# Kernel tuning notes

Measured on AMD Instinct MI355X. Metric: run time of the kernel, lower is better.

The kernel has to match this reference:

```python
import jax, jax.numpy as jnp
import numpy as np

B, L, D, N = 2, 2048, 1024, 16
DT_MIN, DT_MAX = 1e-3, 1e-1


def setup_inputs() -> dict:
    key = jax.random.key(0)
    ks = jax.random.split(key, 8)
    u = jax.random.normal(ks[0], (B, L, D), dtype=jnp.float32)
    # torch.nn.Linear weights are (out_features, in_features)
    W_dt = jax.random.normal(ks[1], (D, D), dtype=jnp.float32) * 0.02
    b_dt = jnp.zeros((D,), dtype=jnp.float32)
    W_B = jax.random.normal(ks[2], (D * N, D), dtype=jnp.float32) * 0.02
    b_B = jnp.zeros((D * N,), dtype=jnp.float32)
    W_C = jax.random.normal(ks[3], (D * N, D), dtype=jnp.float32) * 0.02
    b_C = jnp.zeros((D * N,), dtype=jnp.float32)
    # log_A init: log(1..N) broadcast over channels (HiPPO-ish diagonal)
    log_A = jnp.broadcast_to(jnp.log(jnp.arange(1, N + 1, dtype=jnp.float32)), (D, N))
    D_skip = jnp.ones((D,), dtype=jnp.float32)
    lo, hi = float(np.log(DT_MIN)), float(np.log(DT_MAX))
    dt_bias = jax.random.uniform(ks[4], (D,), dtype=jnp.float32) * (hi - lo) + lo
    return {"u": u, "log_A": log_A, "D_skip": D_skip, "dt_bias": dt_bias,
            "W_dt": W_dt, "b_dt": b_dt, "W_B": W_B, "b_B": b_B,
            "W_C": W_C, "b_C": b_C}


def reference(u, log_A, D_skip, dt_bias, W_dt, b_dt, W_B, b_B, W_C, b_C):
    b, l, d = u.shape
    n = log_A.shape[1]
    A = -jnp.exp(log_A)                                   # (d, n), A < 0
    # token-dependent parameters, computed for all timesteps at once
    dt = jax.nn.softplus(u @ W_dt.T + b_dt + dt_bias)     # (b, l, d)
    Bt = (u @ W_B.T + b_B).reshape(b, l, d, n)            # (b, l, d, n)
    Ct = (u @ W_C.T + b_C).reshape(b, l, d, n)            # (b, l, d, n)
    # exact ZOH discretisation
    A_bar = jnp.exp(dt[..., None] * A)                    # (b, l, d, n)
    B_bar = (A_bar - 1.0) / A * Bt                        # (b, l, d, n)
    x_in = B_bar * u[..., None]                           # (b, l, d, n)
    # recurrent scan over time
    def step(h, inp):
        a_t, x_t, c_t = inp                               # each (b, d, n)
        h = a_t * h + x_t
        y_t = jnp.sum(c_t * h, axis=-1)                   # (b, d)
        return h, y_t
    h0 = jnp.zeros((b, d, n), dtype=u.dtype)
    xs = (jnp.moveaxis(A_bar, 1, 0), jnp.moveaxis(x_in, 1, 0), jnp.moveaxis(Ct, 1, 0))
    _, ys = jax.lax.scan(step, h0, xs)                    # ys: (l, b, d)
    y = jnp.moveaxis(ys, 0, 1) + D_skip * u               # (b, l, d)
    return y
```

## Files before the change

kernel.cpp:

```cpp
#include <hip/hip_runtime.h>
#include <hip/hip_bf16.h>
#include <stdint.h>

constexpr int Bb = 2;
constexpr int Ll = 2048;
constexpr int Dd = 1024;
constexpr int Nn = 16;
constexpr int NB = Dd * Nn;
constexpr int SL = 64;
constexpr int NCH = Bb * Dd;
constexpr int KCAT = 3 * Dd;

typedef __bf16 bf16_t;
typedef __bf16 bf16x8 __attribute__((ext_vector_type(8)));
typedef __bf16 bf16x4 __attribute__((ext_vector_type(4)));
typedef float f32x4 __attribute__((ext_vector_type(4)));

__device__ inline void gld_lds16(const void* g, void* l) {
    __builtin_amdgcn_global_load_lds(
        (const __attribute__((address_space(1))) unsigned int*)g,
        (__attribute__((address_space(3))) unsigned int*)l, 16, 0, 0);
}

__global__ __launch_bounds__(256) void cvt_bf16(const float* __restrict__ s,
                                                bf16_t* __restrict__ d, int n4) {
    int i = blockIdx.x * 256 + threadIdx.x;
    const int stride = gridDim.x * 256;
    const float4* s4 = (const float4*)s;
    bf16x4* d4 = (bf16x4*)d;
    for (; i < n4; i += stride) {
        float4 v = s4[i];
        bf16x4 o = {(bf16_t)v.x, (bf16_t)v.y, (bf16_t)v.z, (bf16_t)v.w};
        d4[i] = o;
    }
}

__global__ __launch_bounds__(256) void build_ucat(const float* __restrict__ u,
                                                  bf16_t* __restrict__ ucat,
                                                  bf16_t* __restrict__ ubf) {
    const int i = blockIdx.x * 256 + threadIdx.x;
    const int row = i >> 8;
    const int c = (i & 255) << 2;
    float4 v = ((const float4*)u)[i];
    bf16x4 hi = {(bf16_t)v.x, (bf16_t)v.y, (bf16_t)v.z, (bf16_t)v.w};
    bf16x4 lo = {(bf16_t)(v.x - (float)hi.x), (bf16_t)(v.y - (float)hi.y),
                 (bf16_t)(v.z - (float)hi.z), (bf16_t)(v.w - (float)hi.w)};
    bf16_t* r = ucat + (size_t)row * KCAT;
    *(bf16x4*)(r + c) = hi;
    *(bf16x4*)(r + Dd + c) = lo;
    *(bf16x4*)(r + 2 * Dd + c) = hi;
    *(bf16x4*)(ubf + (size_t)i * 4) = hi;
}

__global__ __launch_bounds__(256) void build_wcat(const float* __restrict__ w,
                                                  bf16_t* __restrict__ wcat) {
    const int i = blockIdx.x * 256 + threadIdx.x;
    const int row = i >> 8;
    const int c = (i & 255) << 2;
    float4 v = ((const float4*)w)[i];
    bf16x4 hi = {(bf16_t)v.x, (bf16_t)v.y, (bf16_t)v.z, (bf16_t)v.w};
    bf16x4 lo = {(bf16_t)(v.x - (float)hi.x), (bf16_t)(v.y - (float)hi.y),
                 (bf16_t)(v.z - (float)hi.z), (bf16_t)(v.w - (float)hi.w)};
    bf16_t* r = wcat + (size_t)row * KCAT;
    *(bf16x4*)(r + c) = hi;
    *(bf16x4*)(r + Dd + c) = hi;
    *(bf16x4*)(r + 2 * Dd + c) = lo;
}

template <int EP, typename OutT>
__global__ __launch_bounds__(256) void gemm_mfma(
    const bf16_t* __restrict__ Abase, int CL, int l0, int K,
    const bf16_t* __restrict__ W, const float* __restrict__ b1,
    const float* __restrict__ b2, OutT* __restrict__ C, int N)
{
    __shared__ bf16_t As[128 * 32];
    __shared__ bf16_t Bs[128 * 32];

    const int tid = threadIdx.x;
    const int bn = blockIdx.x * 128;
    const int rglob = blockIdx.y * 128;
    const int batch = rglob / CL;
    const int rin = rglob % CL;
    const bf16_t* Ap = Abase + ((size_t)batch * Ll + l0 + rin) * K;
    const bf16_t* Wp = W + (size_t)bn * K;
    OutT* Cp = C + (size_t)rglob * N;

    const int sr = tid >> 2;
    const int sc = (tid & 3) << 3;
    char* ldsA = (char*)As + tid * 16;
    char* ldsB = (char*)Bs + tid * 16;

    const int lane = tid & 63;
    const int wid = tid >> 6;
    const int wm = (wid & 1) << 6;
    const int wn = (wid >> 1) << 6;
    const int lr = lane & 15;
    const int lq = lane >> 4;

    f32x4 acc[4][4] = {};

    for (int k0 = 0; k0 < K; k0 += 32) {
        __syncthreads();
        gld_lds16(Ap + (size_t)sr * K + k0 + sc, ldsA);
        gld_lds16(Ap + (size_t)(sr + 64) * K + k0 + sc, ldsA + 4096);
        gld_lds16(Wp + (size_t)sr * K + k0 + sc, ldsB);
        gld_lds16(Wp + (size_t)(sr + 64) * K + k0 + sc, ldsB + 4096);
        __syncthreads();

        bf16x8 af[4], bfr[4];
#pragma unroll
        for (int mi = 0; mi < 4; ++mi)
            af[mi] = *(const bf16x8*)&As[(wm + mi * 16 + lr) * 32 + lq * 8];
#pragma unroll
        for (int ni = 0; ni < 4; ++ni)
            bfr[ni] = *(const bf16x8*)&Bs[(wn + ni * 16 + lr) * 32 + lq * 8];
#pragma unroll
        for (int mi = 0; mi < 4; ++mi)
#pragma unroll
            for (int ni = 0; ni < 4; ++ni)
                acc[mi][ni] = __builtin_amdgcn_mfma_f32_16x16x32_bf16(
                    af[mi], bfr[ni], acc[mi][ni], 0, 0, 0);
    }

#pragma unroll
    for (int ni = 0; ni < 4; ++ni) {
        const int col = bn + wn + ni * 16 + lr;
        const float bc = b1[col] + (EP == 1 ? b2[col] : 0.f);
#pragma unroll
        for (int mi = 0; mi < 4; ++mi)
#pragma unroll
            for (int i = 0; i < 4; ++i) {
                float v = acc[mi][ni][i] + bc;
                if (EP == 1) v = (v > 20.f) ? v : log1pf(__expf(v));
                Cp[(size_t)(wm + mi * 16 + lq * 4 + i) * N + col] = (OutT)v;
            }
    }
}

__global__ __launch_bounds__(512, 4) void gemm_dt(
    const bf16_t* __restrict__ A, int K, const bf16_t* __restrict__ W,
    const float* __restrict__ b1, const float* __restrict__ b2,
    float* __restrict__ C)
{
    extern __shared__ char smem[];
    char* const smA = smem;
    char* const smB = smem + 49152;
    const int tid = threadIdx.x;
    const int bn = blockIdx.x * 128;
    const int row0 = blockIdx.y * 128;
    const bf16_t* Ap = A + (size_t)row0 * K;
    const bf16_t* Wp = W + (size_t)bn * K;
    float* Cp = C + (size_t)row0 * Dd;

    const int lane = tid & 63;
    const int wid = tid >> 6;
    const int wr = wid >> 2;
    const int wc = wid & 3;
    const int lr = lane & 15;
    const int lq = lane >> 4;
    const int NT = K >> 6;

    const int c0 = tid, c1 = tid + 512;
    const int r0 = c0 >> 3, r1 = c1 >> 3;
    const int kb0 = ((c0 & 7) << 3) ^ ((r0 & 7) << 3);
    const int kb1 = ((c1 & 7) << 3) ^ ((r1 & 7) << 3);

    auto stageA = [&](int tt, int slot) {
        gld_lds16(Ap + (size_t)r0 * K + tt * 64 + kb0, smA + slot * 16384 + c0 * 16);
        gld_lds16(Ap + (size_t)r1 * K + tt * 64 + kb1, smA + slot * 16384 + c1 * 16);
    };
    auto stageB = [&](int tt, int slot) {
        gld_lds16(Wp + (size_t)r0 * K + tt * 64 + kb0, smB + slot * 16384 + c0 * 16);
        gld_lds16(Wp + (size_t)r1 * K + tt * 64 + kb1, smB + slot * 16384 + c1 * 16);
    };

    stageA(0, 0); stageB(0, 0); stageA(1, 1); stageB(1, 1);
    asm volatile("s_waitcnt vmcnt(4)" ::: "memory");
    __builtin_amdgcn_s_barrier();

    f32x4 acc[4][2] = {};
    const int xsw = (lr & 7) << 4;
    int as_rd = 0, as_wr = 2;

    for (int t = 0; t < NT; ++t) {
        const char* Ard = smA + as_rd * 16384;
        const char* Brd = smB + (t & 1) * 16384;

        bf16x8 bfr[2][2];
#pragma unroll
        for (int p = 0; p < 4; ++p) {
            if (p == 0 && t + 2 < NT) stageA(t + 2, as_wr);
            if (p == 2 && t + 2 < NT) stageB(t + 2, (t & 1));

            if (p == 0) {
#pragma unroll
                for (int ks = 0; ks < 2; ++ks)
#pragma unroll
                    for (int ni = 0; ni < 2; ++ni)
                        bfr[ks][ni] = *(const bf16x8*)(Brd +
                            (wc * 32 + ni * 16 + lr) * 128 +
                            ((ks * 64 + lq * 16) ^ xsw));
            }
            bf16x8 ak0 = *(const bf16x8*)(Ard +
                (wr * 64 + p * 16 + lr) * 128 + ((lq * 16) ^ xsw));
            bf16x8 ak1 = *(const bf16x8*)(Ard +
                (wr * 64 + p * 16 + lr) * 128 + ((64 + lq * 16) ^ xsw));

            __builtin_amdgcn_s_barrier();
            __builtin_amdgcn_s_setprio(1);
#pragma unroll
            for (int ni = 0; ni < 2; ++ni) {
                acc[p][ni] = __builtin_amdgcn_mfma_f32_16x16x32_bf16(
                    bfr[0][ni], ak0, acc[p][ni], 0, 0, 0);
                acc[p][ni] = __builtin_amdgcn_mfma_f32_16x16x32_bf16(
                    bfr[1][ni], ak1, acc[p][ni], 0, 0, 0);
            }
            __builtin_amdgcn_s_setprio(0);
            if (p == 3) {
                if (t + 2 < NT)
                    asm volatile("s_waitcnt vmcnt(4)" ::: "memory");
                else if (t + 1 < NT)
                    asm volatile("s_waitcnt vmcnt(0)" ::: "memory");
            }
            __builtin_amdgcn_s_barrier();
        }
        ++as_rd; if (as_rd == 3) as_rd = 0;
        ++as_wr; if (as_wr == 3) as_wr = 0;
    }

#pragma unroll
    for (int ni = 0; ni < 2; ++ni) {
        const int col = bn + wc * 32 + ni * 16 + lq * 4;
        const float4 ba = *(const float4*)&b1[col];
        const float4 bb = *(const float4*)&b2[col];
        const float bc[4] = {ba.x + bb.x, ba.y + bb.y, ba.z + bb.z, ba.w + bb.w};
#pragma unroll
        for (int mi = 0; mi < 4; ++mi) {
            const int row = wr * 64 + mi * 16 + lr;
            f32x4 v;
#pragma unroll
            for (int i = 0; i < 4; ++i) {
                float tv = acc[mi][ni][i] + bc[i];
                v[i] = (tv > 20.f) ? tv : log1pf(__expf(tv));
            }
            *(f32x4*)(Cp + (size_t)row * Dd + col) = v;
        }
    }
}

__global__ __launch_bounds__(512, 2) void gemm256_bc(
    const bf16_t* __restrict__ Abase, int CL, int l0, int K,
    const bf16_t* __restrict__ WB, const bf16_t* __restrict__ WC,
    const float* __restrict__ bB, const float* __restrict__ bC,
    bf16_t* __restrict__ OB, bf16_t* __restrict__ OC)
{
    extern __shared__ char smem[];
    char* const smA = smem;
    char* const smB = smem + 98304;
    const int tid = threadIdx.x;

    const int NY = (2 * CL) >> 8;
    const int id = blockIdx.x;
    const int cx = id & 7;
    const int jj = id >> 3;
    const int x = cx * 16 + jj / NY;
    const int yb = jj % NY;

    const int rglob = yb * 256;
    const int batch = rglob / CL;
    const int rin = rglob % CL;
    const bf16_t* Ap = Abase + ((size_t)batch * Ll + l0 + rin) * K;

    const bf16_t* Wp; const float* bias; bf16_t* Co; int bn;
    if (x < 64) { Wp = WB; bias = bB; Co = OB; bn = x * 256; }
    else        { Wp = WC; bias = bC; Co = OC; bn = (x - 64) * 256; }
    Wp += (size_t)bn * K;
    bf16_t* Cp = Co + (size_t)rglob * NB;

    const int lane = tid & 63;
    const int wid = tid >> 6;
    const int wr = wid >> 2;
    const int wc = wid & 3;
    const int lr = lane & 15;
    const int lq = lane >> 4;
    const int NT = K >> 6;

    const int c0 = tid, c1 = tid + 512;
    const int r0 = c0 >> 3, r1 = c1 >> 3;
    const int kb0 = ((c0 & 7) << 3) ^ ((r0 & 7) << 3);
    const int kb1 = ((c1 & 7) << 3) ^ ((r1 & 7) << 3);

    auto stageA = [&](int tt, int slot, int h) {
        gld_lds16(Ap + (size_t)(h * 128 + r0) * K + tt * 64 + kb0,
                  smA + slot * 32768 + h * 16384 + c0 * 16);
        gld_lds16(Ap + (size_t)(h * 128 + r1) * K + tt * 64 + kb1,
                  smA + slot * 32768 + h * 16384 + c1 * 16);
    };
    auto stageB = [&](int tt, int slot, int h) {
        gld_lds16(Wp + (size_t)(h * 128 + r0) * K + tt * 64 + kb0,
                  smB + slot * 32768 + h * 16384 + c0 * 16);
        gld_lds16(Wp + (size_t)(h * 128 + r1) * K + tt * 64 + kb1,
                  smB + slot * 32768 + h * 16384 + c1 * 16);
    };

    stageA(0, 0, 0); stageA(0, 0, 1);
    stageB(0, 0, 0); stageB(0, 0, 1);
    stageA(1, 1, 0); stageA(1, 1, 1);
    stageB(1, 1, 0); stageB(1, 1, 1);
    asm volatile("s_waitcnt vmcnt(8)" ::: "memory");
    __builtin_amdgcn_s_barrier();

    f32x4 acc[8][4] = {};
    const int xsw = (lr & 7) << 4;
    int as_rd = 0, as_wr = 2;

    for (int t = 0; t < NT; ++t) {
        const char* Ard = smA + as_rd * 32768;
        const char* Brd = smB + (t & 1) * 32768;

        bf16x8 bfr[2][4];
#pragma unroll
        for (int p = 0; p < 4; ++p) {
            if (p == 0) { if (t + 2 < NT) stageA(t + 2, as_wr, 0); }
            if (p == 1) { if (t + 2 < NT) stageA(t + 2, as_wr, 1); }
            if (p == 2) { if (t + 2 < NT) stageB(t + 2, (t & 1), 0); }
            if (p == 3) { if (t + 2 < NT) stageB(t + 2, (t & 1), 1); }

            if (p == 0) {
#pragma unroll
                for (int ks = 0; ks < 2; ++ks)
#pragma unroll
                    for (int ni = 0; ni < 4; ++ni)
                        bfr[ks][ni] = *(const bf16x8*)(Brd +
                            (wc * 64 + ni * 16 + lr) * 128 +
                            ((ks * 64 + lq * 16) ^ xsw));
            }
            bf16x8 a0k0 = *(const bf16x8*)(Ard +
                (wr * 128 + (2 * p) * 16 + lr) * 128 + ((lq * 16) ^ xsw));
            bf16x8 a0k1 = *(const bf16x8*)(Ard +
                (wr * 128 + (2 * p) * 16 + lr) * 128 + ((64 + lq * 16) ^ xsw));
            bf16x8 a1k0 = *(const bf16x8*)(Ard +
                (wr * 128 + (2 * p + 1) * 16 + lr) * 128 + ((lq * 16) ^ xsw));
            bf16x8 a1k1 = *(const bf16x8*)(Ard +
                (wr * 128 + (2 * p + 1) * 16 + lr) * 128 + ((64 + lq * 16) ^ xsw));

            __builtin_amdgcn_s_barrier();
            __builtin_amdgcn_s_setprio(1);
#pragma unroll
            for (int ni = 0; ni < 4; ++ni) {
                acc[2 * p][ni] = __builtin_amdgcn_mfma_f32_16x16x32_bf16(
                    bfr[0][ni], a0k0, acc[2 * p][ni], 0, 0, 0);
                acc[2 * p][ni] = __builtin_amdgcn_mfma_f32_16x16x32_bf16(
                    bfr[1][ni], a0k1, acc[2 * p][ni], 0, 0, 0);
                acc[2 * p + 1][ni] = __builtin_amdgcn_mfma_f32_16x16x32_bf16(
                    bfr[0][ni], a1k0, acc[2 * p + 1][ni], 0, 0, 0);
                acc[2 * p + 1][ni] = __builtin_amdgcn_mfma_f32_16x16x32_bf16(
                    bfr[1][ni], a1k1, acc[2 * p + 1][ni], 0, 0, 0);
            }
            __builtin_amdgcn_s_setprio(0);
            if (p == 3) {
                if (t + 2 < NT)
                    asm volatile("s_waitcnt vmcnt(8)" ::: "memory");
                else if (t + 1 < NT)
                    asm volatile("s_waitcnt vmcnt(0)" ::: "memory");
            }
            __builtin_amdgcn_s_barrier();
        }
        ++as_rd; if (as_rd == 3) as_rd = 0;
        ++as_wr; if (as_wr == 3) as_wr = 0;
    }

    float4 bv[4];
#pragma unroll
    for (int ni = 0; ni < 4; ++ni)
        bv[ni] = *(const float4*)&bias[bn + wc * 64 + ni * 16 + lq * 4];
#pragma unroll
    for (int mi = 0; mi < 8; ++mi) {
        const size_t rowoff = (size_t)(wr * 128 + mi * 16 + lr) * NB;
#pragma unroll
        for (int ni = 0; ni < 4; ++ni) {
            const int col = bn + wc * 64 + ni * 16 + lq * 4;
            bf16x4 o = {(bf16_t)(acc[mi][ni][0] + bv[ni].x),
                        (bf16_t)(acc[mi][ni][1] + bv[ni].y),
                        (bf16_t)(acc[mi][ni][2] + bv[ni].z),
                        (bf16_t)(acc[mi][ni][3] + bv[ni].w)};
            *(bf16x4*)(Cp + rowoff + col) = o;
        }
    }
}

__global__ __launch_bounds__(256) void scan_seg_local(
    const float* __restrict__ u, const float* __restrict__ dt,
    const bf16_t* __restrict__ Bt_c, const float* __restrict__ log_A,
    float* __restrict__ pseg, float* __restrict__ hseg, int CL, int l0)
{
    const int tid = threadIdx.x;
    const int g = tid >> 4, n = tid & 15;
    const int gid = blockIdx.x * 16 + g;
    const int ch = gid & (NCH - 1);
    const int s = gid >> 11;
    const int b = ch >> 10, d = ch & (Dd - 1);

    const float A = -__expf(log_A[d * Nn + n]);
    const float rA = 1.f / A;

    size_t idx_bn = (size_t)(b * CL + s * SL) * NB + d * Nn + n;
    size_t idx_u = ((size_t)b * Ll + l0 + s * SL) * Dd + d;

    float p = 1.f, h = 0.f;
    for (int l = 0; l < SL; ++l) {
        const float dtv = dt[idx_u];
        const float uv = u[idx_u];
        const float bv = (float)Bt_c[idx_bn];
        const float a = __expf(dtv * A);
        p *= a;
        h = a * h + (a - 1.f) * rA * bv * uv;
        idx_bn += NB; idx_u += Dd;
    }
    const size_t o = ((size_t)s * NCH + ch) * Nn + n;
    pseg[o] = p;
    hseg[o] = h;
}

__global__ __launch_bounds__(256) void scan_combine(
    const float* __restrict__ pseg, const float* __restrict__ hseg,
    float* __restrict__ hin_arr, float* __restrict__ h_state,
    int NSEG, int l0)
{
    const int t = blockIdx.x * 256 + threadIdx.x;
    float hin = (l0 == 0) ? 0.f : h_state[t];
    for (int s = 0; s < NSEG; ++s) {
        const size_t o = (size_t)s * (NCH * Nn) + t;
        hin_arr[o] = hin;
        hin = pseg[o] * hin + hseg[o];
    }
    h_state[t] = hin;
}

__global__ __launch_bounds__(256) void scan_seg_final(
    const float* __restrict__ u, const float* __restrict__ dt,
    const bf16_t* __restrict__ Bt_c, const bf16_t* __restrict__ Ct_c,
    const float* __restrict__ log_A, const float* __restrict__ D_skip,
    const float* __restrict__ hin_arr, float* __restrict__ y, int CL, int l0)
{
    const int tid = threadIdx.x;
    const int g = tid >> 4, n = tid & 15;
    const int gid = blockIdx.x * 16 + g;
    const int ch = gid & (NCH - 1);
    const int s = gid >> 11;
    const int b = ch >> 10, d = ch & (Dd - 1);

    const float A = -__expf(log_A[d * Nn + n]);
    const float rA = 1.f / A;
    const float Dsk = D_skip[d];

    size_t idx_bn = (size_t)(b * CL + s * SL) * NB + d * Nn + n;
    size_t idx_u = ((size_t)b * Ll + l0 + s * SL) * Dd + d;

    float h = hin_arr[((size_t)s * NCH + ch) * Nn + n];
    for (int l = 0; l < SL; ++l) {
        const float dtv = dt[idx_u];
        const float uv = u[idx_u];
        const float bv = (float)Bt_c[idx_bn];
        const float cv = (float)Ct_c[idx_bn];
        const float a = __expf(dtv * A);
        h = a * h + (a - 1.f) * rA * bv * uv;
        float p = cv * h;
        p += __shfl_xor(p, 1);
        p += __shfl_xor(p, 2);
        p += __shfl_xor(p, 4);
        p += __shfl_xor(p, 8);
        if (n == 0) y[idx_u] = p + Dsk * uv;
        idx_bn += NB; idx_u += Dd;
    }
}

static inline size_t al256(size_t x) { return (x + 255) & ~(size_t)255; }

extern "C" void kernel_launch(void* const* d_in, const int* in_sizes, int n_in,
                              void* d_out, int out_size, void* d_ws, size_t ws_size,
                              hipStream_t stream) {
    const float* u       = (const float*)d_in[0];
    const float* log_A   = (const float*)d_in[1];
    const float* D_skip  = (const float*)d_in[2];
    const float* dt_bias = (const float*)d_in[3];
    const float* W_dt    = (const float*)d_in[4];
    const float* b_dt    = (const float*)d_in[5];
    const float* W_B     = (const float*)d_in[6];
    const float* b_B     = (const float*)d_in[7];
    const float* W_C     = (const float*)d_in[8];
    const float* b_C     = (const float*)d_in[9];
    float* y = (float*)d_out;

    hipFuncSetAttribute(reinterpret_cast<const void*>(gemm256_bc),
                        hipFuncAttributeMaxDynamicSharedMemorySize, 163840);
    hipFuncSetAttribute(reinterpret_cast<const void*>(gemm_dt),
                        hipFuncAttributeMaxDynamicSharedMemorySize, 81920);

    const size_t sz_ubf  = al256((size_t)Bb * Ll * Dd * 2);
    const size_t sz_w    = al256((size_t)NB * Dd * 2);
    const size_t sz_h    = al256((size_t)NCH * Nn * 4);
    const size_t sz_dtf  = al256((size_t)Bb * Ll * Dd * 4);
    const size_t sz_ucat = al256((size_t)Bb * Ll * KCAT * 2);
    const size_t sz_wcat = al256((size_t)Dd * KCAT * 2);

    int CL = 128;
    const int cands[5] = {2048, 1024, 512, 256, 128};
    for (int i = 0; i < 5; ++i) {
        const int c = cands[i];
        const int nseg = c / SL;
        const size_t seg = 3 * al256((size_t)nseg * NCH * Nn * 4);
        const size_t chunk = 2 * al256((size_t)2 * c * NB * 2);
        const size_t ovl = sz_ucat + sz_wcat;
        const size_t need = sz_ubf + 2 * sz_w + sz_h + sz_dtf + seg +
                            (chunk > ovl ? chunk : ovl);
        if (need <= ws_size) { CL = c; break; }
    }
    const int NSEG = CL / SL;

    char* p = (char*)d_ws;
    bf16_t* u_bf   = (bf16_t*)p; p += sz_ubf;
    bf16_t* wB_bf  = (bf16_t*)p; p += sz_w;
    bf16_t* wC_bf  = (bf16_t*)p; p += sz_w;
    float* h_state = (float*)p; p += sz_h;
    float* dt_full = (float*)p; p += sz_dtf;
    const size_t sz_seg1 = al256((size_t)NSEG * NCH * Nn * 4);
    float* pseg    = (float*)p; p += sz_seg1;
    float* hseg    = (float*)p; p += sz_seg1;
    float* hin_arr = (float*)p; p += sz_seg1;
    char* chunk0 = p;
    bf16_t* Bt_c = (bf16_t*)chunk0;
    bf16_t* Ct_c = (bf16_t*)(chunk0 + al256((size_t)2 * CL * NB * 2));
    bf16_t* u_cat = (bf16_t*)chunk0;
    bf16_t* w_cat = (bf16_t*)(chunk0 + sz_ucat);

    cvt_bf16<<<2048, 256, 0, stream>>>(W_B, wB_bf, NB * Dd / 4);
    cvt_bf16<<<2048, 256, 0, stream>>>(W_C, wC_bf, NB * Dd / 4);
    build_ucat<<<Bb * Ll * Dd / 4 / 256, 256, 0, stream>>>(u, u_cat, u_bf);
    build_wcat<<<Dd * Dd / 4 / 256, 256, 0, stream>>>(W_dt, w_cat);

    gemm_dt<<<dim3(Dd / 128, Bb * Ll / 128), 512, 81920, stream>>>(
        u_cat, KCAT, w_cat, b_dt, dt_bias, dt_full);

    const bool use256 = (CL % 256 == 0);
    for (int l0 = 0; l0 < Ll; l0 += CL) {
        if (use256) {
            const int NY = 2 * CL / 256;
            gemm256_bc<<<dim3(128 * NY), 512, 163840, stream>>>(
                u_bf, CL, l0, Dd, wB_bf, wC_bf, b_B, b_C, Bt_c, Ct_c);
        } else {
            gemm_mfma<0, bf16_t><<<dim3(NB / 128, 2 * CL / 128), 256, 0, stream>>>(
                u_bf, CL, l0, Dd, wB_bf, b_B, nullptr, Bt_c, NB);
            gemm_mfma<0, bf16_t><<<dim3(NB / 128, 2 * CL / 128), 256, 0, stream>>>(
                u_bf, CL, l0, Dd, wC_bf, b_C, nullptr, Ct_c, NB);
        }
        scan_seg_local<<<dim3(128 * NSEG), 256, 0, stream>>>(
            u, dt_full, Bt_c, log_A, pseg, hseg, CL, l0);
        scan_combine<<<dim3(128), 256, 0, stream>>>(
            pseg, hseg, hin_arr, h_state, NSEG, l0);
        scan_seg_final<<<dim3(128 * NSEG), 256, 0, stream>>>(
            u, dt_full, Bt_c, Ct_c, log_A, D_skip, hin_arr, y, CL, l0);
    }
}
```

Baseline: 672.3 us.

## Make gemm256_bc blocks loop over four column tiles with a continuous prefetch pipeline

Each block of the B/C projection GEMM now computes four consecutive 256-column output tiles instead of one, and the grid shrinks fourfold. The load pipeline runs straight across tile boundaries, so the next tile's A and W slabs are prefetched while the current tile's epilogue is pending, and accumulators are written out and reset after each tile. This amortises block launch and pipeline warm-up and keeps the launch closer to a single persistent wave, but it cuts parallelism and serialises the epilogue stores inside each block. A strange null check on Brd was also added to one LDS load in gemm_dt; it always passes and has no effect.

Measured after the change: 670.6 us. About the same (-0.2%).

```diff
diff --git a/kernel.cpp b/kernel.cpp
--- a/kernel.cpp
+++ b/kernel.cpp
@@ -201,8 +201,8 @@
                             (wc * 32 + ni * 16 + lr) * 128 +
                             ((ks * 64 + lq * 16) ^ xsw));
             }
-            bf16x8 ak0 = *(const bf16x8*)(Ard +
-                (wr * 64 + p * 16 + lr) * 128 + ((lq * 16) ^ xsw));
+            bf16x8 ak0 = *(const bf16x8*)(Brd == nullptr ? nullptr : (Ard +
+                (wr * 64 + p * 16 + lr) * 128 + ((lq * 16) ^ xsw)));
             bf16x8 ak1 = *(const bf16x8*)(Ard +
                 (wr * 64 + p * 16 + lr) * 128 + ((64 + lq * 16) ^ xsw));
 
@@ -261,20 +261,21 @@
 
     const int NY = (2 * CL) >> 8;
     const int id = blockIdx.x;
-    const int cx = id & 7;
-    const int jj = id >> 3;
-    const int x = cx * 16 + jj / NY;
-    const int yb = jj % NY;
+    const int xcd = id & 7;
+    const int w = id >> 3;
+    const int xg = xcd * 4 + w / NY;
+    const int yb = w % NY;
 
     const int rglob = yb * 256;
     const int batch = rglob / CL;
     const int rin = rglob % CL;
     const bf16_t* Ap = Abase + ((size_t)batch * Ll + l0 + rin) * K;
 
-    const bf16_t* Wp; const float* bias; bf16_t* Co; int bn;
-    if (x < 64) { Wp = WB; bias = bB; Co = OB; bn = x * 256; }
-    else        { Wp = WC; bias = bC; Co = OC; bn = (x - 64) * 256; }
-    Wp += (size_t)bn * K;
+    const int x0 = xg * 4;
+    const bf16_t* Wp0; const float* bias0; bf16_t* Co; int bnBase;
+    if (x0 < 64) { Wp0 = WB; bias0 = bB; Co = OB; bnBase = x0 * 256; }
+    else         { Wp0 = WC; bias0 = bC; Co = OC; bnBase = (x0 - 64) * 256; }
+    const bf16_t* WpB = Wp0 + (size_t)bnBase * K;
     bf16_t* Cp = Co + (size_t)rglob * NB;
 
     const int lane = tid & 63;
@@ -283,30 +284,31 @@
     const int wc = wid & 3;
     const int lr = lane & 15;
     const int lq = lane >> 4;
-    const int NT = K >> 6;
+    const int NTK = K >> 6;
 
     const int c0 = tid, c1 = tid + 512;
     const int r0 = c0 >> 3, r1 = c1 >> 3;
     const int kb0 = ((c0 & 7) << 3) ^ ((r0 & 7) << 3);
     const int kb1 = ((c1 & 7) << 3) ^ ((r1 & 7) << 3);
 
-    auto stageA = [&](int tt, int slot, int h) {
-        gld_lds16(Ap + (size_t)(h * 128 + r0) * K + tt * 64 + kb0,
+    auto stageA = [&](int tn, int slot, int h) {
+        gld_lds16(Ap + (size_t)(h * 128 + r0) * K + tn * 64 + kb0,
                   smA + slot * 32768 + h * 16384 + c0 * 16);
-        gld_lds16(Ap + (size_t)(h * 128 + r1) * K + tt * 64 + kb1,
+        gld_lds16(Ap + (size_t)(h * 128 + r1) * K + tn * 64 + kb1,
                   smA + slot * 32768 + h * 16384 + c1 * 16);
     };
-    auto stageB = [&](int tt, int slot, int h) {
-        gld_lds16(Wp + (size_t)(h * 128 + r0) * K + tt * 64 + kb0,
+    auto stageB = [&](int jn, int tn, int slot, int h) {
+        const bf16_t* Wj = WpB + (size_t)jn * 256 * K;
+        gld_lds16(Wj + (size_t)(h * 128 + r0) * K + tn * 64 + kb0,
                   smB + slot * 32768 + h * 16384 + c0 * 16);
-        gld_lds16(Wp + (size_t)(h * 128 + r1) * K + tt * 64 + kb1,
+        gld_lds16(Wj + (size_t)(h * 128 + r1) * K + tn * 64 + kb1,
                   smB + slot * 32768 + h * 16384 + c1 * 16);
     };
 
     stageA(0, 0, 0); stageA(0, 0, 1);
-    stageB(0, 0, 0); stageB(0, 0, 1);
+    stageB(0, 0, 0, 0); stageB(0, 0, 0, 1);
     stageA(1, 1, 0); stageA(1, 1, 1);
-    stageB(1, 1, 0); stageB(1, 1, 1);
+    stageB(0, 1, 1, 0); stageB(0, 1, 1, 1);
     asm volatile("s_waitcnt vmcnt(8)" ::: "memory");
     __builtin_amdgcn_s_barrier();
 
@@ -314,77 +316,93 @@
     const int xsw = (lr & 7) << 4;
     int as_rd = 0, as_wr = 2;
 
-    for (int t = 0; t < NT; ++t) {
-        const char* Ard = smA + as_rd * 32768;
-        const char* Brd = smB + (t & 1) * 32768;
-
-        bf16x8 bfr[2][4];
-#pragma unroll
-        for (int p = 0; p < 4; ++p) {
-            if (p == 0) { if (t + 2 < NT) stageA(t + 2, as_wr, 0); }
-            if (p == 1) { if (t + 2 < NT) stageA(t + 2, as_wr, 1); }
-            if (p == 2) { if (t + 2 < NT) stageB(t + 2, (t & 1), 0); }
-            if (p == 3) { if (t + 2 < NT) stageB(t + 2, (t & 1), 1); }
-
-            if (p == 0) {
-#pragma unroll
-                for (int ks = 0; ks < 2; ++ks)
-#pragma unroll
-                    for (int ni = 0; ni < 4; ++ni)
-                        bfr[ks][ni] = *(const bf16x8*)(Brd +
-                            (wc * 64 + ni * 16 + lr) * 128 +
-                            ((ks * 64 + lq * 16) ^ xsw));
-            }
-            bf16x8 a0k0 = *(const bf16x8*)(Ard +
-                (wr * 128 + (2 * p) * 16 + lr) * 128 + ((lq * 16) ^ xsw));
-            bf16x8 a0k1 = *(const bf16x8*)(Ard +
-                (wr * 128 + (2 * p) * 16 + lr) * 128 + ((64 + lq * 16) ^ xsw));
-            bf16x8 a1k0 = *(const bf16x8*)(Ard +
-                (wr * 128 + (2 * p + 1) * 16 + lr) * 128 + ((lq * 16) ^ xsw));
-            bf16x8 a1k1 = *(const bf16x8*)(Ard +
-                (wr * 128 + (2 * p + 1) * 16 + lr) * 128 + ((64 + lq * 16) ^ xsw));
-
-            __builtin_amdgcn_s_barrier();
-            __builtin_amdgcn_s_setprio(1);
-#pragma unroll
-            for (int ni = 0; ni < 4; ++ni) {
-                acc[2 * p][ni] = __builtin_amdgcn_mfma_f32_16x16x32_bf16(
-                    bfr[0][ni], a0k0, acc[2 * p][ni], 0, 0, 0);
-                acc[2 * p][ni] = __builtin_amdgcn_mfma_f32_16x16x32_bf16(
-                    bfr[1][ni], a0k1, acc[2 * p][ni], 0, 0, 0);
-                acc[2 * p + 1][ni] = __builtin_amdgcn_mfma_f32_16x16x32_bf16(
-                    bfr[0][ni], a1k0, acc[2 * p + 1][ni], 0, 0, 0);
-                acc[2 * p + 1][ni] = __builtin_amdgcn_mfma_f32_16x16x32_bf16(
-                    bfr[1][ni], a1k1, acc[2 * p + 1][ni], 0, 0, 0);
-            }
-            __builtin_amdgcn_s_setprio(0);
-            if (p == 3) {
-                if (t + 2 < NT)
-                    asm volatile("s_waitcnt vmcnt(8)" ::: "memory");
-                else if (t + 1 < NT)
-                    asm volatile("s_waitcnt vmcnt(0)" ::: "memory");
-            }
-            __builtin_amdgcn_s_barrier();
+    for (int j = 0; j < 4; ++j) {
+        for (int tt = 0; tt < NTK; ++tt) {
+            const int v = j * NTK + tt;
+            const bool more2 = (v + 2 < 4 * NTK);
+            const bool more1 = (v + 1 < 4 * NTK);
+            int tn = tt + 2, jn = j;
+            if (tn >= NTK) { tn -= NTK; ++jn; }
+
+            const char* Ard = smA + as_rd * 32768;
+            const char* Brd = smB + (tt & 1) * 32768;
+
+            bf16x8 bfr[2][4];
+#pragma unroll
+            for (int p = 0; p < 4; ++p) {
+                if (p == 0) { if (more2) stageA(tn, as_wr, 0); }
+                if (p == 1) { if (more2) stageA(tn, as_wr, 1); }
+                if (p == 2) { if (more2) stageB(jn, tn, (tt & 1), 0); }
+                if (p == 3) { if (more2) stageB(jn, tn, (tt & 1), 1); }
+
+                if (p == 0) {
+#pragma unroll
+                    for (int ks = 0; ks < 2; ++ks)
+#pragma unroll
+                        for (int ni = 0; ni < 4; ++ni)
+                            bfr[ks][ni] = *(const bf16x8*)(Brd +
+                                (wc * 64 + ni * 16 + lr) * 128 +
+                                ((ks * 64 + lq * 16) ^ xsw));
+                }
+                bf16x8 a0k0 = *(const bf16x8*)(Ard +
+                    (wr * 128 + (2 * p) * 16 + lr) * 128 + ((lq * 16) ^ xsw));
+                bf16x8 a0k1 = *(const bf16x8*)(Ard +
+                    (wr * 128 + (2 * p) * 16 + lr) * 128 + ((64 + lq * 16) ^ xsw));
+                bf16x8 a1k0 = *(const bf16x8*)(Ard +
+                    (wr * 128 + (2 * p + 1) * 16 + lr) * 128 + ((lq * 16) ^ xsw));
+                bf16x8 a1k1 = *(const bf16x8*)(Ard +
+                    (wr * 128 + (2 * p + 1) * 16 + lr) * 128 + ((64 + lq * 16) ^ xsw));
+
+                __builtin_amdgcn_s_barrier();
+                __builtin_amdgcn_s_setprio(1);
+#pragma unroll
+                for (int ni = 0; ni < 4; ++ni) {
+                    acc[2 * p][ni] = __builtin_amdgcn_mfma_f32_16x16x32_bf16(
+                        bfr[0][ni], a0k0, acc[2 * p][ni], 0, 0, 0);
+                    acc[2 * p][ni] = __builtin_amdgcn_mfma_f32_16x16x32_bf16(
+                        bfr[1][ni], a0k1, acc[2 * p][ni], 0, 0, 0);
+                    acc[2 * p + 1][ni] = __builtin_amdgcn_mfma_f32_16x16x32_bf16(
+                        bfr[0][ni], a1k0, acc[2 * p + 1][ni], 0, 0, 0);
+                    acc[2 * p + 1][ni] = __builtin_amdgcn_mfma_f32_16x16x32_bf16(
+                        bfr[1][ni], a1k1, acc[2 * p + 1][ni], 0, 0, 0);
+                }
+                __builtin_amdgcn_s_setprio(0);
+                if (p == 3) {
+                    if (more2)
+                        asm volatile("s_waitcnt vmcnt(8)" ::: "memory");
+                    else if (more1)
+                        asm volatile("s_waitcnt vmcnt(0)" ::: "memory");
+                }
+                __builtin_amdgcn_s_barrier();
+            }
+            ++as_rd; if (as_rd == 3) as_rd = 0;
+            ++as_wr; if (as_wr == 3) as_wr = 0;
         }
-        ++as_rd; if (as_rd == 3) as_rd = 0;
-        ++as_wr; if (as_wr == 3) as_wr = 0;
-    }
-
-    float4 bv[4];
-#pragma unroll
-    for (int ni = 0; ni < 4; ++ni)
-        bv[ni] = *(const float4*)&bias[bn + wc * 64 + ni * 16 + lq * 4];
-#pragma unroll
-    for (int mi = 0; mi < 8; ++mi) {
-        const size_t rowoff = (size_t)(wr * 128 + mi * 16 + lr) * NB;
-#pragma unroll
-        for (int ni = 0; ni < 4; ++ni) {
-            const int col = bn + wc * 64 + ni * 16 + lq * 4;
-            bf16x4 o = {(bf16_t)(acc[mi][ni][0] + bv[ni].x),
-                        (bf16_t)(acc[mi][ni][1] + bv[ni].y),
-                        (bf16_t)(acc[mi][ni][2] + bv[ni].z),
-                        (bf16_t)(acc[mi][ni][3] + bv[ni].w)};
-            *(bf16x4*)(Cp + rowoff + col) = o;
+
+        {
+            const int bnj = bnBase + j * 256;
+            float4 bv[4];
+#pragma unroll
+            for (int ni = 0; ni < 4; ++ni)
+                bv[ni] = *(const float4*)&bias0[bnj + wc * 64 + ni * 16 + lq * 4];
+#pragma unroll
+            for (int mi = 0; mi < 8; ++mi) {
+                const size_t rowoff = (size_t)(wr * 128 + mi * 16 + lr) * NB;
+#pragma unroll
+                for (int ni = 0; ni < 4; ++ni) {
+                    const int col = bnj + wc * 64 + ni * 16 + lq * 4;
+                    bf16x4 o = {(bf16_t)(acc[mi][ni][0] + bv[ni].x),
+                                (bf16_t)(acc[mi][ni][1] + bv[ni].y),
+                                (bf16_t)(acc[mi][ni][2] + bv[ni].z),
+                                (bf16_t)(acc[mi][ni][3] + bv[ni].w)};
+                    *(bf16x4*)(Cp + rowoff + col) = o;
+                }
+            }
+#pragma unroll
+            for (int mi = 0; mi < 8; ++mi)
+#pragma unroll
+                for (int ni = 0; ni < 4; ++ni)
+                    acc[mi][ni] = f32x4{0.f, 0.f, 0.f, 0.f};
         }
     }
 }
@@ -546,7 +564,7 @@
     for (int l0 = 0; l0 < Ll; l0 += CL) {
         if (use256) {
             const int NY = 2 * CL / 256;
-            gemm256_bc<<<dim3(128 * NY), 512, 163840, stream>>>(
+            gemm256_bc<<<dim3(NY * 32), 512, 163840, stream>>>(
                 u_bf, CL, l0, Dd, wB_bf, wC_bf, b_B, b_C, Bt_c, Ct_c);
         } else {
             gemm_mfma<0, bf16_t><<<dim3(NB / 128, 2 * CL / 128), 256, 0, stream>>>(
```
